# Performance work log

Hardware: AMD Instinct MI355X
Metric: run time of the kernel (lower is better)

Reference implementation:

```python
import jax, jax.numpy as jnp
import numpy as np
import math

NUM_HEADS = 8
HEAD_SIZE = 32

def get_alibi_slopes(n_heads):
    def pow2_slopes(n):
        start = 2.0 ** (-2.0 ** (-(math.log2(n) - 3)))
        ratio = start
        return [start * ratio ** i for i in range(n)]
    if math.log2(n_heads).is_integer():
        return np.array(pow2_slopes(n_heads), dtype=np.float32)
    cp2 = 2 ** math.floor(math.log2(n_heads))
    extra = pow2_slopes(2 * cp2)[0::2][: n_heads - cp2]
    return np.array(pow2_slopes(cp2) + extra, dtype=np.float32)

ALIBI_SLOPES = jnp.asarray(get_alibi_slopes(NUM_HEADS))  # [H]

def setup_inputs() -> dict:
    key = jax.random.key(0)
    ks = jax.random.split(key, 6)
    B, T, C = 32, 512, 256
    s = 1.0 / math.sqrt(C)
    return {
        "x": jax.random.normal(ks[0], (B, T, C), dtype=jnp.float32),
        "Wq": jax.random.normal(ks[1], (C, NUM_HEADS * HEAD_SIZE), dtype=jnp.float32) * s,
        "Wk": jax.random.normal(ks[2], (C, NUM_HEADS * HEAD_SIZE), dtype=jnp.float32) * s,
        "Wv": jax.random.normal(ks[3], (C, NUM_HEADS * HEAD_SIZE), dtype=jnp.float32) * s,
        "Wo": jax.random.normal(ks[4], (NUM_HEADS * HEAD_SIZE, C), dtype=jnp.float32) * s,
        "bo": jax.random.normal(ks[5], (C,), dtype=jnp.float32) * 0.01,
    }

def reference(x, Wq, Wk, Wv, Wo, bo):
    # Faithful eval-mode forward (dropout disabled) of the torch MultiHeadAttention.
    B, T, C = x.shape
    H, D = NUM_HEADS, HEAD_SIZE
    q = (x @ Wq).reshape(B, T, H, D).transpose(0, 2, 1, 3)  # [B,H,T,D]
    k = (x @ Wk).reshape(B, T, H, D).transpose(0, 2, 1, 3)
    v = (x @ Wv).reshape(B, T, H, D).transpose(0, 2, 1, 3)
    scale = 1.0 / math.sqrt(D)
    wei = jnp.einsum("bhtd,bhsd->bhts", q, k) * scale  # [B,H,T,T]
    pos = jnp.arange(T)
    rel = (pos[None, :] - pos[:, None]).astype(jnp.float32)  # bias[i,j] = j - i
    bias = ALIBI_SLOPES[:, None, None] * rel[None, :, :]      # [H,T,T]
    wei = wei + bias[None]
    causal = pos[None, :] <= pos[:, None]  # [T,T], True where j <= i
    wei = jnp.where(causal[None, None], wei, -jnp.inf)
    wei = jax.nn.softmax(wei, axis=-1)
    out = jnp.einsum("bhts,bhsd->bhtd", wei, v)  # [B,H,T,D]
    out = out.transpose(0, 2, 1, 3).reshape(B, T, H * D)
    return out @ Wo + bo
```

## Files before the change

### kernel.cpp

```cpp
#include <hip/hip_runtime.h>
#include <stdint.h>

#define LOG2E 1.4426950408889634f
#define QSCALE_LN2 0.25506068f

typedef __attribute__((ext_vector_type(8))) short bf16x8;
typedef __attribute__((ext_vector_type(4))) float f32x4;

__device__ __forceinline__ unsigned short f2bf(float f) {
  union { float f; unsigned int u; } v; v.f = f;
  unsigned int u = v.u;
  u += 0x7FFFu + ((u >> 16) & 1u);
  return (unsigned short)(u >> 16);
}

__device__ __forceinline__ unsigned int cvt_pk_bf16(float lo, float hi) {
  unsigned int r;
  asm("v_cvt_pk_bf16_f32 %0, %1, %2" : "=v"(r) : "v"(lo), "v"(hi));
  return r;
}

struct WPtrs { const float* src[4]; unsigned short* dst[4]; };
__global__ void transpose_w(WPtrs p) {
  __shared__ float tile[32][33];
  const float* src = p.src[blockIdx.z];
  unsigned short* dst = p.dst[blockIdx.z];
  int x = blockIdx.x * 32 + threadIdx.x;
  int y = blockIdx.y * 32 + threadIdx.y;
  #pragma unroll
  for (int j = 0; j < 32; j += 8)
    tile[threadIdx.y + j][threadIdx.x] = src[(y + j) * 256 + x];
  __syncthreads();
  int xo = blockIdx.y * 32 + threadIdx.x;
  int yo = blockIdx.x * 32 + threadIdx.y;
  #pragma unroll
  for (int j = 0; j < 32; j += 8)
    dst[(yo + j) * 256 + xo] = f2bf(tile[threadIdx.x][threadIdx.y + j]);
}

__launch_bounds__(256, 3)
__global__ void gemm_qkv(const float* __restrict__ Ax,
                         const unsigned short* __restrict__ Wt,
                         unsigned short* __restrict__ q_out,
                         unsigned short* __restrict__ k_out,
                         unsigned short* __restrict__ vT) {
  __shared__ unsigned short As[64][72];
  __shared__ unsigned short Bs[256][72];
  const int tid = threadIdx.x;
  const int m0 = blockIdx.x * 64;
  const int wsel = blockIdx.y;
  const unsigned short* W = Wt + wsel * 65536;
  const int w = tid >> 6, lane = tid & 63;
  const int n0 = w * 64;
  const int lr = lane & 15, lg = lane >> 4;

  f32x4 acc[4][4] = {};

  for (int kt = 0; kt < 4; ++kt) {
    #pragma unroll
    for (int i = 0; i < 2; ++i) {
      int c = tid + i * 256;
      int row = c >> 3, colg = c & 7;
      const float* s = &Ax[(size_t)(m0 + row) * 256 + kt * 64 + colg * 8];
      float4 f0 = *reinterpret_cast<const float4*>(s);
      float4 f1 = *reinterpret_cast<const float4*>(s + 4);
      uint4 pk;
      pk.x = cvt_pk_bf16(f0.x, f0.y); pk.y = cvt_pk_bf16(f0.z, f0.w);
      pk.z = cvt_pk_bf16(f1.x, f1.y); pk.w = cvt_pk_bf16(f1.z, f1.w);
      *reinterpret_cast<uint4*>(&As[row][colg * 8]) = pk;
    }
    #pragma unroll
    for (int i = 0; i < 8; ++i) {
      int c = tid + i * 256;
      int row = c >> 3, colg = c & 7;
      *reinterpret_cast<int4*>(&Bs[row][colg * 8]) =
        *reinterpret_cast<const int4*>(&W[(size_t)row * 256 + kt * 64 + colg * 8]);
    }
    __syncthreads();
    #pragma unroll
    for (int kk = 0; kk < 2; ++kk) {
      bf16x8 af[4], bfr[4];
      #pragma unroll
      for (int mf = 0; mf < 4; ++mf)
        af[mf] = *reinterpret_cast<const bf16x8*>(&As[mf * 16 + lr][kk * 32 + lg * 8]);
      #pragma unroll
      for (int nf = 0; nf < 4; ++nf)
        bfr[nf] = *reinterpret_cast<const bf16x8*>(&Bs[n0 + nf * 16 + lr][kk * 32 + lg * 8]);
      #pragma unroll
      for (int mf = 0; mf < 4; ++mf)
        #pragma unroll
        for (int nf = 0; nf < 4; ++nf)
          acc[mf][nf] = __builtin_amdgcn_mfma_f32_16x16x32_bf16(af[mf], bfr[nf], acc[mf][nf], 0, 0, 0);
    }
    __syncthreads();
  }

  if (wsel < 2) {
    unsigned short* dst = (wsel == 0) ? q_out : k_out;
    const float qs = (wsel == 0) ? QSCALE_LN2 : 1.0f;
    #pragma unroll
    for (int mf = 0; mf < 4; ++mf)
      #pragma unroll
      for (int nf = 0; nf < 4; ++nf)
        #pragma unroll
        for (int r = 0; r < 4; ++r)
          dst[(size_t)(m0 + mf * 16 + lg * 4 + r) * 256 + (n0 + nf * 16 + lr)] =
            f2bf(acc[mf][nf][r] * qs);
  } else {
    #pragma unroll
    for (int mf = 0; mf < 4; ++mf)
      #pragma unroll
      for (int nf = 0; nf < 4; ++nf) {
        int ncol = n0 + nf * 16 + lr;
        int h = ncol >> 5, d = ncol & 31;
        int m = m0 + mf * 16 + lg * 4;
        int b = m >> 9, t = m & 511;
        ushort4 pk;
        pk.x = f2bf(acc[mf][nf][0]); pk.y = f2bf(acc[mf][nf][1]);
        pk.z = f2bf(acc[mf][nf][2]); pk.w = f2bf(acc[mf][nf][3]);
        *reinterpret_cast<ushort4*>(&vT[((size_t)((b * 8 + h) * 32 + d)) * 512 + t]) = pk;
      }
  }
}

__launch_bounds__(256, 3)
__global__ void gemm_out(const unsigned short* __restrict__ Ab,
                         const unsigned short* __restrict__ W,
                         const float* __restrict__ bo,
                         float* __restrict__ f_out) {
  __shared__ unsigned short As[128][72];
  __shared__ unsigned short Bs[128][72];
  const int tid = threadIdx.x;
  const int m0 = blockIdx.x * 128;
  const int n0 = blockIdx.y * 128;
  const int w = tid >> 6, lane = tid & 63;
  const int wm = (w >> 1) * 64, wn = (w & 1) * 64;
  const int lr = lane & 15, lg = lane >> 4;

  f32x4 acc[4][4] = {};

  for (int kt = 0; kt < 4; ++kt) {
    #pragma unroll
    for (int cc = 0; cc < 4; ++cc) {
      int c = tid + cc * 256;
      int row = c >> 3, colg = c & 7;
      *reinterpret_cast<int4*>(&As[row][colg * 8]) =
        *reinterpret_cast<const int4*>(&Ab[(size_t)(m0 + row) * 256 + kt * 64 + colg * 8]);
      *reinterpret_cast<int4*>(&Bs[row][colg * 8]) =
        *reinterpret_cast<const int4*>(&W[(size_t)(n0 + row) * 256 + kt * 64 + colg * 8]);
    }
    __syncthreads();
    #pragma unroll
    for (int kk = 0; kk < 2; ++kk) {
      bf16x8 af[4], bfr[4];
      #pragma unroll
      for (int mf = 0; mf < 4; ++mf)
        af[mf] = *reinterpret_cast<const bf16x8*>(&As[wm + mf * 16 + lr][kk * 32 + lg * 8]);
      #pragma unroll
      for (int nf = 0; nf < 4; ++nf)
        bfr[nf] = *reinterpret_cast<const bf16x8*>(&Bs[wn + nf * 16 + lr][kk * 32 + lg * 8]);
      #pragma unroll
      for (int mf = 0; mf < 4; ++mf)
        #pragma unroll
        for (int nf = 0; nf < 4; ++nf)
          acc[mf][nf] = __builtin_amdgcn_mfma_f32_16x16x32_bf16(af[mf], bfr[nf], acc[mf][nf], 0, 0, 0);
    }
    __syncthreads();
  }

  #pragma unroll
  for (int mf = 0; mf < 4; ++mf)
    #pragma unroll
    for (int nf = 0; nf < 4; ++nf)
      #pragma unroll
      for (int r = 0; r < 4; ++r) {
        int ncol = n0 + wn + nf * 16 + lr;
        f_out[(size_t)(m0 + wm + mf * 16 + lg * 4 + r) * 256 + ncol] = acc[mf][nf][r] + bo[ncol];
      }
}

struct CSt {
  bf16x8 qf;
  f32x4 o0, o1;
  float m, l, bb0;
  int nfull, qq;
};

__device__ __forceinline__ void attn_init(CSt& st, int c, const unsigned short* qb,
    int b, int h, int lr, int lg, float slope2) {
  st.qq = c * 16;
  st.qf = *reinterpret_cast<const bf16x8*>(
      &qb[(size_t)(b * 512 + st.qq + lr) * 256 + h * 32 + lg * 8]);
  f32x4 z = {0.f, 0.f, 0.f, 0.f};
  st.o0 = z; st.o1 = z;
  st.m = -1e30f; st.l = 0.f;
  st.nfull = (st.qq >= 63) ? ((st.qq - 63) / 64 + 1) : 0;
  st.bb0 = slope2 * (float)(lg * 4 - lr - st.qq);
}

__device__ __forceinline__ void attn_step(CSt& st, int s,
    const bf16x8* kf, const bf16x8* vf, char* __restrict__ Pw,
    int lr, int lg, float slope2, const float* cc, int swz) {
  const int kb0 = s * 64;
  f32x4 sv[4];
  __builtin_amdgcn_s_setprio(1);
  #pragma unroll
  for (int t = 0; t < 4; ++t) {
    f32x4 z = {0.f, 0.f, 0.f, 0.f};
    sv[t] = __builtin_amdgcn_mfma_f32_16x16x32_bf16(kf[t], st.qf, z, 0, 0, 0);
  }
  __builtin_amdgcn_s_setprio(0);
  float bb = st.bb0 + slope2 * (float)kb0;
  float x[16];
  #pragma unroll
  for (int t = 0; t < 4; ++t)
    #pragma unroll
    for (int r = 0; r < 4; ++r)
      x[t * 4 + r] = sv[t][r] + (bb + cc[t * 4 + r]);
  if (s >= st.nfull) {
    int thr = st.qq + lr - kb0 - lg * 4;
    #pragma unroll
    for (int t = 0; t < 4; ++t)
      #pragma unroll
      for (int r = 0; r < 4; ++r)
        x[t * 4 + r] = ((t * 16 + r) <= thr) ? x[t * 4 + r] : -1e30f;
  }
  float bm = x[0];
  #pragma unroll
  for (int j = 1; j < 16; ++j) bm = fmaxf(bm, x[j]);
  bm = fmaxf(bm, __shfl_xor(bm, 16));
  bm = fmaxf(bm, __shfl_xor(bm, 32));
  float mn = fmaxf(st.m, bm);
  float alpha = __builtin_amdgcn_exp2f(st.m - mn);
  st.m = mn;
  st.l *= alpha;
  #pragma unroll
  for (int r = 0; r < 4; ++r) { st.o0[r] *= alpha; st.o1[r] *= alpha; }
  float ps = 0.f;
  #pragma unroll
  for (int j = 0; j < 16; ++j) { x[j] = __builtin_amdgcn_exp2f(x[j] - mn); ps += x[j]; }
  st.l += ps;
  char* Prow = Pw + lr * 256;
  #pragma unroll
  for (int t = 0; t < 4; ++t)
    #pragma unroll
    for (int pp = 0; pp < 2; ++pp) {
      unsigned int w2 = cvt_pk_bf16(x[t * 4 + 2 * pp], x[t * 4 + 2 * pp + 1]);
      *reinterpret_cast<unsigned int*>(Prow + ((t * 32 + lg * 8 + pp * 4) ^ swz)) = w2;
    }
  __builtin_amdgcn_s_setprio(1);
  #pragma unroll
  for (int ks = 0; ks < 2; ++ks) {
    bf16x8 pb = *reinterpret_cast<const bf16x8*>(Prow + ((ks * 64 + lg * 16) ^ swz));
    st.o0 = __builtin_amdgcn_mfma_f32_16x16x32_bf16(vf[ks * 2 + 0], pb, st.o0, 0, 0, 0);
    st.o1 = __builtin_amdgcn_mfma_f32_16x16x32_bf16(vf[ks * 2 + 1], pb, st.o1, 0, 0, 0);
  }
  __builtin_amdgcn_s_setprio(0);
}

__device__ __forceinline__ void attn_step2(CSt& st, int s, bool maskB,
    const bf16x8* kf, const bf16x8* vf, char* __restrict__ Pw,
    int lr, int lg, float slope2, const float* cc, int swz) {
  const int kb0 = s * 64;
  f32x4 sv[8];
  __builtin_amdgcn_s_setprio(1);
  #pragma unroll
  for (int t = 0; t < 8; ++t) {
    f32x4 z = {0.f, 0.f, 0.f, 0.f};
    sv[t] = __builtin_amdgcn_mfma_f32_16x16x32_bf16(kf[t], st.qf, z, 0, 0, 0);
  }
  __builtin_amdgcn_s_setprio(0);
  const float bbA = st.bb0 + slope2 * (float)kb0;
  const float bbB = bbA + slope2 * 64.0f;
  float x[32];
  #pragma unroll
  for (int t = 0; t < 4; ++t)
    #pragma unroll
    for (int r = 0; r < 4; ++r) {
      x[t * 4 + r]      = sv[t][r]     + (bbA + cc[t * 4 + r]);
      x[16 + t * 4 + r] = sv[4 + t][r] + (bbB + cc[t * 4 + r]);
    }
  if (maskB) {
    int thr = st.qq + lr - (kb0 + 64) - lg * 4;
    #pragma unroll
    for (int t = 0; t < 4; ++t)
      #pragma unroll
      for (int r = 0; r < 4; ++r)
        x[16 + t * 4 + r] = ((t * 16 + r) <= thr) ? x[16 + t * 4 + r] : -1e30f;
  }
  float bm = x[0];
  #pragma unroll
  for (int j = 1; j < 32; ++j) bm = fmaxf(bm, x[j]);
  bm = fmaxf(bm, __shfl_xor(bm, 16));
  bm = fmaxf(bm, __shfl_xor(bm, 32));
  float mn = fmaxf(st.m, bm);
  float alpha = __builtin_amdgcn_exp2f(st.m - mn);
  st.m = mn;
  st.l *= alpha;
  #pragma unroll
  for (int r = 0; r < 4; ++r) { st.o0[r] *= alpha; st.o1[r] *= alpha; }
  float ps = 0.f;
  #pragma unroll
  for (int j = 0; j < 32; ++j) { x[j] = __builtin_amdgcn_exp2f(x[j] - mn); ps += x[j]; }
  st.l += ps;
  char* Prow = Pw + lr * 256;
  #pragma unroll
  for (int t = 0; t < 4; ++t)
    #pragma unroll
    for (int pp = 0; pp < 2; ++pp) {
      const int cb = (t * 32 + lg * 8 + pp * 4) ^ swz;
      *reinterpret_cast<unsigned int*>(Prow + cb) =
          cvt_pk_bf16(x[t * 4 + 2 * pp], x[t * 4 + 2 * pp + 1]);
      *reinterpret_cast<unsigned int*>(Prow + 128 + cb) =
          cvt_pk_bf16(x[16 + t * 4 + 2 * pp], x[16 + t * 4 + 2 * pp + 1]);
    }
  __builtin_amdgcn_s_setprio(1);
  #pragma unroll
  for (int ks = 0; ks < 4; ++ks) {
    const int cb = (ks >> 1) * 128 + ((((ks & 1) * 64) + lg * 16) ^ swz);
    bf16x8 pb = *reinterpret_cast<const bf16x8*>(Prow + cb);
    st.o0 = __builtin_amdgcn_mfma_f32_16x16x32_bf16(vf[ks * 2 + 0], pb, st.o0, 0, 0, 0);
    st.o1 = __builtin_amdgcn_mfma_f32_16x16x32_bf16(vf[ks * 2 + 1], pb, st.o1, 0, 0, 0);
  }
  __builtin_amdgcn_s_setprio(0);
}

__device__ __forceinline__ void attn_fin(CSt& st, unsigned short* __restrict__ ob,
                                         int b, int h, int lr, int lg) {
  float l = st.l;
  l += __shfl_xor(l, 16);
  l += __shfl_xor(l, 32);
  float inv = 1.0f / l;
  unsigned int w0 = cvt_pk_bf16(st.o0[0] * inv, st.o0[1] * inv);
  unsigned int w1 = cvt_pk_bf16(st.o0[2] * inv, st.o0[3] * inv);
  unsigned int w2 = cvt_pk_bf16(st.o1[0] * inv, st.o1[1] * inv);
  unsigned int w3 = cvt_pk_bf16(st.o1[2] * inv, st.o1[3] * inv);
  size_t obase = (size_t)(b * 512 + st.qq + lr) * 256 + h * 32;
  *reinterpret_cast<uint2*>(&ob[obase + lg * 4]) = make_uint2(w0, w1);
  *reinterpret_cast<uint2*>(&ob[obase + 16 + lg * 4]) = make_uint2(w2, w3);
}

__device__ __forceinline__ void chunk_phase(CSt& st, int s, int nc,
    const bf16x8* kf, const bf16x8* vf, char* Pw,
    int lr, int lg, float slope2, const float* cc, int swz) {
  if (s >= nc) return;
  if (s + 1 < nc)
    attn_step2(st, s, (s + 2 >= nc), kf, vf, Pw, lr, lg, slope2, cc, swz);
  else
    attn_step(st, s, kf, vf, Pw, lr, lg, slope2, cc, swz);
}

__launch_bounds__(512)
__global__ void attn_k(const unsigned short* __restrict__ qb,
                       const unsigned short* __restrict__ kb,
                       const unsigned short* __restrict__ vT,
                       unsigned short* __restrict__ ob) {
  __shared__ unsigned short Ks[512 * 32];
  __shared__ unsigned short Vs[32 * 512];
  __shared__ char Pb[32768];
  const int h = blockIdx.x, b = blockIdx.y;
  const int tid = threadIdx.x, wv = tid >> 6, lane = tid & 63;
  const int lr = lane & 15, lg = lane >> 4;

  {
    const unsigned short* ksrc = kb + ((size_t)b * 512) * 256 + h * 32;
    #pragma unroll
    for (int it = 0; it < 4; ++it) {
      int idx = tid + it * 512;
      int row = idx >> 2, g = idx & 3;
      int gs = g ^ ((row >> 1) & 3);
      *reinterpret_cast<int4*>(&Ks[row * 32 + gs * 8]) =
        *reinterpret_cast<const int4*>(&ksrc[(size_t)row * 256 + g * 8]);
    }
    const unsigned short* vsrc = vT + ((size_t)(b * 8 + h) * 32) * 512;
    #pragma unroll
    for (int it = 0; it < 4; ++it) {
      int idx = tid + it * 512;
      int d = idx >> 6, cg = idx & 63;
      int col = (cg * 8) ^ ((d & 7) << 3);
      *reinterpret_cast<int4*>(&Vs[d * 512 + col]) =
        *reinterpret_cast<const int4*>(&vsrc[(size_t)d * 512 + cg * 8]);
    }
  }
  __syncthreads();

  const float slope2 = exp2f(-(float)(h + 1)) * LOG2E;
  float cc[16];
  #pragma unroll
  for (int t = 0; t < 4; ++t)
    #pragma unroll
    for (int r = 0; r < 4; ++r) cc[t * 4 + r] = slope2 * (float)(t * 16 + r);
  const int swz = (lr & 7) << 4;
  const int kchunk = (lg ^ ((lr >> 1) & 3)) * 8;
  char* Pw = Pb + wv * 4096;

  const int g = wv;
  const int c0 = g, c1 = 15 - g, c2 = 16 + g, c3 = 31 - g;
  CSt s0, s1, s2, s3;
  attn_init(s0, c0, qb, b, h, lr, lg, slope2);
  attn_init(s1, c1, qb, b, h, lr, lg, slope2);
  attn_init(s2, c2, qb, b, h, lr, lg, slope2);
  attn_init(s3, c3, qb, b, h, lr, lg, slope2);
  const int n0 = c0 / 4 + 1, n1 = c1 / 4 + 1, n2 = c2 / 4 + 1, n3 = c3 / 4 + 1;

  for (int s = 0; s < n3; s += 2) {
    const int kb0 = s * 64;
    bf16x8 kf[8], vf[8];
    #pragma unroll
    for (int t = 0; t < 8; ++t)
      kf[t] = *reinterpret_cast<const bf16x8*>(&Ks[(kb0 + t * 16 + lr) * 32 + kchunk]);
    #pragma unroll
    for (int ks = 0; ks < 4; ++ks)
      #pragma unroll
      for (int dt = 0; dt < 2; ++dt) {
        int d = dt * 16 + lr;
        int col = (kb0 + ks * 32 + lg * 8) ^ ((d & 7) << 3);
        vf[ks * 2 + dt] = *reinterpret_cast<const bf16x8*>(&Vs[d * 512 + col]);
      }
    chunk_phase(s0, s, n0, kf, vf, Pw, lr, lg, slope2, cc, swz);
    chunk_phase(s1, s, n1, kf, vf, Pw, lr, lg, slope2, cc, swz);
    chunk_phase(s2, s, n2, kf, vf, Pw, lr, lg, slope2, cc, swz);
    chunk_phase(s3, s, n3, kf, vf, Pw, lr, lg, slope2, cc, swz);
  }

  attn_fin(s0, ob, b, h, lr, lg);
  attn_fin(s1, ob, b, h, lr, lg);
  attn_fin(s2, ob, b, h, lr, lg);
  attn_fin(s3, ob, b, h, lr, lg);
}

extern "C" void kernel_launch(void* const* d_in, const int* in_sizes, int n_in,
                              void* d_out, int out_size, void* d_ws, size_t ws_size,
                              hipStream_t stream) {
  const float* x  = (const float*)d_in[0];
  const float* Wq = (const float*)d_in[1];
  const float* Wk = (const float*)d_in[2];
  const float* Wv = (const float*)d_in[3];
  const float* Wo = (const float*)d_in[4];
  const float* bo = (const float*)d_in[5];
  float* out = (float*)d_out;

  char* ws = (char*)d_ws;
  unsigned short* qb = (unsigned short*)(ws);
  unsigned short* kb = (unsigned short*)(ws + (8u  << 20));
  unsigned short* vT = (unsigned short*)(ws + (16u << 20));
  unsigned short* ob = (unsigned short*)(ws + (24u << 20));
  unsigned short* wt = (unsigned short*)(ws + (32u << 20));

  WPtrs p;
  p.src[0] = Wq; p.src[1] = Wk; p.src[2] = Wv; p.src[3] = Wo;
  p.dst[0] = wt; p.dst[1] = wt + 65536; p.dst[2] = wt + 2 * 65536; p.dst[3] = wt + 3 * 65536;
  transpose_w<<<dim3(8, 8, 4), dim3(32, 8), 0, stream>>>(p);

  gemm_qkv<<<dim3(256, 3), 256, 0, stream>>>(x, wt, qb, kb, vT);
  attn_k<<<dim3(8, 32), 512, 0, stream>>>(qb, kb, vT, ob);
  gemm_out<<<dim3(128, 2), 256, 0, stream>>>(ob, wt + 3 * 65536, bo, out);
}
```

Before: 53.75 us.

## Double attention block to 16 waves with two query chunks per wave

The attention kernel launches 1024 threads (16 waves) per batch-head block instead of 8 waves. Each wave now handles two balanced query chunks instead of four, and the per-wave P scratch buffer in shared memory doubles in total size. V fragments are now loaded from shared memory inside each step rather than preloaded into registers per iteration. This cuts register pressure and increases parallelism within the block, at the cost of redundant V LDS reads and higher shared-memory usage.

```diff
diff --git a/kernel.cpp b/kernel.cpp
--- a/kernel.cpp
+++ b/kernel.cpp
@@ -199,7 +199,7 @@
 }
 
 __device__ __forceinline__ void attn_step(CSt& st, int s,
-    const bf16x8* kf, const bf16x8* vf, char* __restrict__ Pw,
+    const bf16x8* kf, const unsigned short* __restrict__ Vs, char* __restrict__ Pw,
     int lr, int lg, float slope2, const float* cc, int swz) {
   const int kb0 = s * 64;
   f32x4 sv[4];
@@ -252,14 +252,20 @@
   #pragma unroll
   for (int ks = 0; ks < 2; ++ks) {
     bf16x8 pb = *reinterpret_cast<const bf16x8*>(Prow + ((ks * 64 + lg * 16) ^ swz));
-    st.o0 = __builtin_amdgcn_mfma_f32_16x16x32_bf16(vf[ks * 2 + 0], pb, st.o0, 0, 0, 0);
-    st.o1 = __builtin_amdgcn_mfma_f32_16x16x32_bf16(vf[ks * 2 + 1], pb, st.o1, 0, 0, 0);
+    #pragma unroll
+    for (int dt = 0; dt < 2; ++dt) {
+      int d = dt * 16 + lr;
+      int col = (kb0 + ks * 32 + lg * 8) ^ ((d & 7) << 3);
+      bf16x8 vfr = *reinterpret_cast<const bf16x8*>(&Vs[d * 512 + col]);
+      if (dt == 0) st.o0 = __builtin_amdgcn_mfma_f32_16x16x32_bf16(vfr, pb, st.o0, 0, 0, 0);
+      else         st.o1 = __builtin_amdgcn_mfma_f32_16x16x32_bf16(vfr, pb, st.o1, 0, 0, 0);
+    }
   }
   __builtin_amdgcn_s_setprio(0);
 }
 
 __device__ __forceinline__ void attn_step2(CSt& st, int s, bool maskB,
-    const bf16x8* kf, const bf16x8* vf, char* __restrict__ Pw,
+    const bf16x8* kf, const unsigned short* __restrict__ Vs, char* __restrict__ Pw,
     int lr, int lg, float slope2, const float* cc, int swz) {
   const int kb0 = s * 64;
   f32x4 sv[8];
@@ -319,8 +325,14 @@
   for (int ks = 0; ks < 4; ++ks) {
     const int cb = (ks >> 1) * 128 + ((((ks & 1) * 64) + lg * 16) ^ swz);
     bf16x8 pb = *reinterpret_cast<const bf16x8*>(Prow + cb);
-    st.o0 = __builtin_amdgcn_mfma_f32_16x16x32_bf16(vf[ks * 2 + 0], pb, st.o0, 0, 0, 0);
-    st.o1 = __builtin_amdgcn_mfma_f32_16x16x32_bf16(vf[ks * 2 + 1], pb, st.o1, 0, 0, 0);
+    #pragma unroll
+    for (int dt = 0; dt < 2; ++dt) {
+      int d = dt * 16 + lr;
+      int col = (kb0 + ks * 32 + lg * 8) ^ ((d & 7) << 3);
+      bf16x8 vfr = *reinterpret_cast<const bf16x8*>(&Vs[d * 512 + col]);
+      if (dt == 0) st.o0 = __builtin_amdgcn_mfma_f32_16x16x32_bf16(vfr, pb, st.o0, 0, 0, 0);
+      else         st.o1 = __builtin_amdgcn_mfma_f32_16x16x32_bf16(vfr, pb, st.o1, 0, 0, 0);
+    }
   }
   __builtin_amdgcn_s_setprio(0);
 }
@@ -341,23 +353,23 @@
 }
 
 __device__ __forceinline__ void chunk_phase(CSt& st, int s, int nc,
-    const bf16x8* kf, const bf16x8* vf, char* Pw,
+    const bf16x8* kf, const unsigned short* __restrict__ Vs, char* Pw,
     int lr, int lg, float slope2, const float* cc, int swz) {
   if (s >= nc) return;
   if (s + 1 < nc)
-    attn_step2(st, s, (s + 2 >= nc), kf, vf, Pw, lr, lg, slope2, cc, swz);
+    attn_step2(st, s, (s + 2 >= nc), kf, Vs, Pw, lr, lg, slope2, cc, swz);
   else
-    attn_step(st, s, kf, vf, Pw, lr, lg, slope2, cc, swz);
-}
-
-__launch_bounds__(512)
+    attn_step(st, s, kf, Vs, Pw, lr, lg, slope2, cc, swz);
+}
+
+__launch_bounds__(1024)
 __global__ void attn_k(const unsigned short* __restrict__ qb,
                        const unsigned short* __restrict__ kb,
                        const unsigned short* __restrict__ vT,
                        unsigned short* __restrict__ ob) {
   __shared__ unsigned short Ks[512 * 32];
   __shared__ unsigned short Vs[32 * 512];
-  __shared__ char Pb[32768];
+  __shared__ char Pb[65536];
   const int h = blockIdx.x, b = blockIdx.y;
   const int tid = threadIdx.x, wv = tid >> 6, lane = tid & 63;
   const int lr = lane & 15, lg = lane >> 4;
@@ -365,8 +377,8 @@
   {
     const unsigned short* ksrc = kb + ((size_t)b * 512) * 256 + h * 32;
     #pragma unroll
-    for (int it = 0; it < 4; ++it) {
-      int idx = tid + it * 512;
+    for (int it = 0; it < 2; ++it) {
+      int idx = tid + it * 1024;
       int row = idx >> 2, g = idx & 3;
       int gs = g ^ ((row >> 1) & 3);
       *reinterpret_cast<int4*>(&Ks[row * 32 + gs * 8]) =
@@ -374,8 +386,8 @@
     }
     const unsigned short* vsrc = vT + ((size_t)(b * 8 + h) * 32) * 512;
     #pragma unroll
-    for (int it = 0; it < 4; ++it) {
-      int idx = tid + it * 512;
+    for (int it = 0; it < 2; ++it) {
+      int idx = tid + it * 1024;
       int d = idx >> 6, cg = idx & 63;
       int col = (cg * 8) ^ ((d & 7) << 3);
       *reinterpret_cast<int4*>(&Vs[d * 512 + col]) =
@@ -395,38 +407,24 @@
   char* Pw = Pb + wv * 4096;
 
   const int g = wv;
-  const int c0 = g, c1 = 15 - g, c2 = 16 + g, c3 = 31 - g;
-  CSt s0, s1, s2, s3;
-  attn_init(s0, c0, qb, b, h, lr, lg, slope2);
-  attn_init(s1, c1, qb, b, h, lr, lg, slope2);
-  attn_init(s2, c2, qb, b, h, lr, lg, slope2);
-  attn_init(s3, c3, qb, b, h, lr, lg, slope2);
-  const int n0 = c0 / 4 + 1, n1 = c1 / 4 + 1, n2 = c2 / 4 + 1, n3 = c3 / 4 + 1;
-
-  for (int s = 0; s < n3; s += 2) {
+  const int cA = g, cB = 31 - g;
+  CSt A, B;
+  attn_init(A, cA, qb, b, h, lr, lg, slope2);
+  attn_init(B, cB, qb, b, h, lr, lg, slope2);
+  const int nA = cA / 4 + 1, nB = cB / 4 + 1;
+
+  for (int s = 0; s < nB; s += 2) {
     const int kb0 = s * 64;
-    bf16x8 kf[8], vf[8];
+    bf16x8 kf[8];
     #pragma unroll
     for (int t = 0; t < 8; ++t)
       kf[t] = *reinterpret_cast<const bf16x8*>(&Ks[(kb0 + t * 16 + lr) * 32 + kchunk]);
-    #pragma unroll
-    for (int ks = 0; ks < 4; ++ks)
-      #pragma unroll
-      for (int dt = 0; dt < 2; ++dt) {
-        int d = dt * 16 + lr;
-        int col = (kb0 + ks * 32 + lg * 8) ^ ((d & 7) << 3);
-        vf[ks * 2 + dt] = *reinterpret_cast<const bf16x8*>(&Vs[d * 512 + col]);
-      }
-    chunk_phase(s0, s, n0, kf, vf, Pw, lr, lg, slope2, cc, swz);
-    chunk_phase(s1, s, n1, kf, vf, Pw, lr, lg, slope2, cc, swz);
-    chunk_phase(s2, s, n2, kf, vf, Pw, lr, lg, slope2, cc, swz);
-    chunk_phase(s3, s, n3, kf, vf, Pw, lr, lg, slope2, cc, swz);
-  }
-
-  attn_fin(s0, ob, b, h, lr, lg);
-  attn_fin(s1, ob, b, h, lr, lg);
-  attn_fin(s2, ob, b, h, lr, lg);
-  attn_fin(s3, ob, b, h, lr, lg);
+    chunk_phase(A, s, nA, kf, Vs, Pw, lr, lg, slope2, cc, swz);
+    chunk_phase(B, s, nB, kf, Vs, Pw, lr, lg, slope2, cc, swz);
+  }
+
+  attn_fin(A, ob, b, h, lr, lg);
+  attn_fin(B, ob, b, h, lr, lg);
 }
 
 extern "C" void kernel_launch(void* const* d_in, const int* in_sizes, int n_in,
@@ -453,6 +451,6 @@
   transpose_w<<<dim3(8, 8, 4), dim3(32, 8), 0, stream>>>(p);
 
   gemm_qkv<<<dim3(256, 3), 256, 0, stream>>>(x, wt, qb, kb, vT);
-  attn_k<<<dim3(8, 32), 512, 0, stream>>>(qb, kb, vT, ob);
+  attn_k<<<dim3(8, 32), 1024, 0, stream>>>(qb, kb, vT, ob);
   gemm_out<<<dim3(128, 2), 256, 0, stream>>>(ob, wt + 3 * 65536, bo, out);
 }
```

Result: slower. 64.11 us (+19.3%).
